# Kernel tuning notes

Hardware: AMD Instinct MI355X
Metric: run time of the kernel (lower is better)

## Reference

```python
import jax, jax.numpy as jnp
import numpy as np

EMBED_DIM = 1024
NUM_HEADS = 16
HEAD_DIM = EMBED_DIM // NUM_HEADS
SCALE = HEAD_DIM ** (-0.5)


def setup_inputs() -> dict:
    key = jax.random.key(0)
    ks = jax.random.split(key, 8)
    B, Nq, Nkv, C = 2, 2048, 2048, EMBED_DIM
    s = C ** (-0.5)
    return {
        "q": jax.random.normal(ks[0], (B, Nq, C), dtype=jnp.float32),
        "kv": jax.random.normal(ks[1], (B, Nkv, C), dtype=jnp.float32),
        "w_q": jax.random.normal(ks[2], (C, C), dtype=jnp.float32) * s,
        "b_q": jnp.zeros((C,), dtype=jnp.float32),
        "w_kv": jax.random.normal(ks[3], (C, 2 * C), dtype=jnp.float32) * s,
        "b_kv": jnp.zeros((2 * C,), dtype=jnp.float32),
        "w_out": jax.random.normal(ks[4], (C, C), dtype=jnp.float32) * s,
        "b_out": jnp.zeros((C,), dtype=jnp.float32),
    }


def reference(q, kv, w_q, b_q, w_kv, b_kv, w_out, b_out):
    B, Nq, C = q.shape
    _, Nkv, _ = kv.shape
    H, D = NUM_HEADS, HEAD_DIM

    # q projection: (B, Nq, C) -> (B, H, Nq, D)
    qp = (q @ w_q + b_q).reshape(B, Nq, H, D).transpose(0, 2, 1, 3)

    # kv projection: (B, Nkv, 2C) -> (2, B, H, Nkv, D); '(two h d)' layout
    kvp = (kv @ w_kv + b_kv).reshape(B, Nkv, 2, H, D).transpose(2, 0, 3, 1, 4)
    kp, vp = kvp[0], kvp[1]

    # attention scores (B, H, Nq, Nkv), softmax over kv axis
    attn = jnp.einsum("bhqd,bhkd->bhqk", qp, kp) * SCALE
    attn = jax.nn.softmax(attn, axis=-1)

    out = jnp.einsum("bhqk,bhkd->bhqd", attn, vp)
    out = out.transpose(0, 2, 1, 3).reshape(B, Nq, C)
    return out @ w_out + b_out
```

## Files before the change

kernel.cpp:

```cpp
#include <hip/hip_runtime.h>

#define NUM_HEADS 16
#define HEAD_DIM 64
#define EMBED 1024
#define SPLIT 2

typedef __attribute__((ext_vector_type(8))) short short8;
typedef __attribute__((ext_vector_type(4))) short short4v;
typedef __attribute__((ext_vector_type(4))) float f32x4;

#if __has_builtin(__builtin_amdgcn_exp2f)
#define EXP2F(x) __builtin_amdgcn_exp2f(x)
#else
#define EXP2F(x) exp2f(x)
#endif

__device__ __forceinline__ f32x4 mfma16_bf16(short4v a, short4v b, f32x4 c) {
#if defined(__HIP_DEVICE_COMPILE__)
  return __builtin_amdgcn_mfma_f32_16x16x16bf16_1k(a, b, c, 0, 0, 0);
#else
  return c;
#endif
}

__device__ __forceinline__ short f2bf(float f) {
  unsigned u = __builtin_bit_cast(unsigned, f);
  u += 0x7fffu + ((u >> 16) & 1u);
  return (short)(u >> 16);
}

__device__ __forceinline__ short f2bf_trunc(float f) {
  return (short)(__builtin_bit_cast(unsigned, f) >> 16);
}

__device__ __forceinline__ void gload_lds16(const void* g, void* l) {
  __builtin_amdgcn_global_load_lds(
      (const __attribute__((address_space(1))) void*)g,
      (__attribute__((address_space(3))) void*)l,
      16, 0, 0);
}

__device__ __forceinline__ void tr_body(const float* __restrict__ in,
                                        short* __restrict__ out, int R, int C,
                                        int bx, int by, float (*t)[33], int tid) {
  int tx = tid & 31, ty = tid >> 5;
#pragma unroll
  for (int i = 0; i < 32; i += 8)
    t[ty + i][tx] = in[(size_t)(by + ty + i) * C + bx + tx];
  __syncthreads();
#pragma unroll
  for (int i = 0; i < 32; i += 8)
    out[(size_t)(bx + ty + i) * R + by + tx] = f2bf(t[tx][ty + i]);
}

__global__ void prep(const float* __restrict__ q, short* __restrict__ q_bf,
                     const float* __restrict__ kv, short* __restrict__ kv_bf,
                     const float* __restrict__ w_q, short* __restrict__ wqt,
                     const float* __restrict__ w_kv, short* __restrict__ wkvt,
                     const float* __restrict__ w_out, short* __restrict__ wot) {
  __shared__ float t[32][33];
  int bid = blockIdx.x, tid = threadIdx.x;
  if (bid < 4096) {
    const float* in = bid < 2048 ? q : kv;
    short* out = bid < 2048 ? q_bf : kv_bf;
    int i = ((bid & 2047) * 256 + tid) * 8;
    float4 f0 = *(const float4*)(in + i);
    float4 f1 = *(const float4*)(in + i + 4);
    short8 r;
    r[0] = f2bf(f0.x); r[1] = f2bf(f0.y); r[2] = f2bf(f0.z); r[3] = f2bf(f0.w);
    r[4] = f2bf(f1.x); r[5] = f2bf(f1.y); r[6] = f2bf(f1.z); r[7] = f2bf(f1.w);
    *(short8*)(out + i) = r;
  } else if (bid < 5120) {
    int r = bid - 4096;
    tr_body(w_q, wqt, 1024, 1024, (r & 31) * 32, (r >> 5) * 32, t, tid);
  } else if (bid < 7168) {
    int r = bid - 5120;
    tr_body(w_kv, wkvt, 1024, 2048, (r & 63) * 32, (r >> 6) * 32, t, tid);
  } else {
    int r = bid - 7168;
    tr_body(w_out, wot, 1024, 1024, (r & 31) * 32, (r >> 5) * 32, t, tid);
  }
}

template <int MODE>
__device__ __forceinline__ void gemm_body(const short* __restrict__ A,
                                          const short* __restrict__ Bt,
                                          const float* __restrict__ bias,
                                          void* __restrict__ Cptr, int N, int K,
                                          int m0, int n0, float scale) {
  __shared__ short As[128 * 32];
  __shared__ short Bs[128 * 32];
  const int tid = threadIdx.x;
  const int wave = tid >> 6, lane = tid & 63;
  const int quad = lane >> 4, l16 = lane & 15;
  const int wr = wave >> 1, wc = wave & 1;

  f32x4 acc[4][4];
#pragma unroll
  for (int i = 0; i < 4; i++)
#pragma unroll
    for (int j = 0; j < 4; j++) acc[i][j] = (f32x4)0.f;

  const int c0 = wave * 2, c1 = wave * 2 + 1;
  const int rowA0 = c0 * 16 + (lane >> 2);
  const int rowA1 = c1 * 16 + (lane >> 2);
  const int kecol = (lane & 3) * 8;

  for (int k0 = 0; k0 < K; k0 += 32) {
    __syncthreads();
    gload_lds16(A + (size_t)(m0 + rowA0) * K + k0 + kecol, (char*)As + c0 * 1024);
    gload_lds16(A + (size_t)(m0 + rowA1) * K + k0 + kecol, (char*)As + c1 * 1024);
    gload_lds16(Bt + (size_t)(n0 + rowA0) * K + k0 + kecol, (char*)Bs + c0 * 1024);
    gload_lds16(Bt + (size_t)(n0 + rowA1) * K + k0 + kecol, (char*)Bs + c1 * 1024);
    __syncthreads();
    short8 a[4], b[4];
#pragma unroll
    for (int i = 0; i < 4; i++)
      a[i] = *(const short8*)(As + (wr * 64 + i * 16 + l16) * 32 + quad * 8);
#pragma unroll
    for (int j = 0; j < 4; j++)
      b[j] = *(const short8*)(Bs + (wc * 64 + j * 16 + l16) * 32 + quad * 8);
#pragma unroll
    for (int i = 0; i < 4; i++)
#pragma unroll
      for (int j = 0; j < 4; j++)
        acc[i][j] = __builtin_amdgcn_mfma_f32_16x16x32_bf16(a[i], b[j], acc[i][j], 0, 0, 0);
  }

#pragma unroll
  for (int j = 0; j < 4; j++) {
    int col = n0 + wc * 64 + j * 16 + l16;
    float bv = bias[col];
    if (MODE == 2) {
      int vcol = col - 1024;
      int h = vcol >> 6, d = vcol & 63;
#pragma unroll
      for (int i = 0; i < 4; i++) {
        int rbase = m0 + wr * 64 + i * 16 + quad * 4;
        int b = rbase >> 11;
        int kvr = rbase & 2047;
        short pk[4];
#pragma unroll
        for (int r = 0; r < 4; r++) pk[r] = f2bf(acc[i][j][r] + bv);
        *(uint2*)((short*)Cptr + ((size_t)(b * 16 + h) * 64 + d) * 2048 + kvr) =
            *(uint2*)pk;
      }
    } else {
#pragma unroll
      for (int i = 0; i < 4; i++) {
        int rbase = m0 + wr * 64 + i * 16 + quad * 4;
#pragma unroll
        for (int r = 0; r < 4; r++) {
          float v = (acc[i][j][r] + bv) * scale;
          if (MODE == 1)
            ((float*)Cptr)[(size_t)(rbase + r) * N + col] = v;
          else
            ((short*)Cptr)[(size_t)(rbase + r) * N + col] = f2bf(v);
        }
      }
    }
  }
}

__global__ __launch_bounds__(256)
void gemm_qkv(const short* __restrict__ q_bf, const short* __restrict__ kv_bf,
              const short* __restrict__ wqt, const short* __restrict__ wkvt,
              const float* __restrict__ b_q, const float* __restrict__ b_kv,
              short* __restrict__ qp, short* __restrict__ kvp,
              short* __restrict__ vt) {
  int y = blockIdx.y;
  int m0 = blockIdx.x * 128;
  if (y < 8) {
    gemm_body<0>(q_bf, wqt, b_q, qp, 1024, 1024, m0, y * 128, 0.125f);
  } else if (y < 16) {
    gemm_body<0>(kv_bf, wkvt, b_kv, kvp, 2048, 1024, m0, (y - 8) * 128, 1.f);
  } else {
    gemm_body<2>(kv_bf, wkvt, b_kv, vt, 2048, 1024, m0, (y - 8) * 128, 1.f);
  }
}

__global__ __launch_bounds__(256)
void gemm_out(const short* __restrict__ A, const short* __restrict__ Bt,
              const float* __restrict__ bias, float* __restrict__ C) {
  gemm_body<1>(A, Bt, bias, C, 1024, 1024, blockIdx.x * 128, blockIdx.y * 128, 1.f);
}

__global__ __launch_bounds__(256)
void attn7(const short* __restrict__ qp, const short* __restrict__ kvp,
           const short* __restrict__ vt, float* __restrict__ opart,
           float* __restrict__ lpart, int B, int Nq, int Nkv) {
  __shared__ short Ks0[64 * 64], Ks1[64 * 64];
  __shared__ short Vs0[64 * 64], Vs1[64 * 64];

  const int tid = threadIdx.x;
  const int wave = tid >> 6, lane = tid & 63;
  const int quad = lane >> 4, l16 = lane & 15;
  const int bh = blockIdx.y;
  const int b = bh >> 4, h = bh & 15;
  const int q0 = blockIdx.x * 64;
  const int z = blockIdx.z;
  const int kvlen = Nkv / SPLIT;
  const int kv_begin = z * kvlen;
  const int niter = kvlen / 64;

  const int qrow = q0 + wave * 16 + l16;
  const short* qbase = qp + ((size_t)b * Nq + qrow) * EMBED + h * HEAD_DIM;
  short8 aq0 = *(const short8*)(qbase + quad * 8);
  short8 aq1 = *(const short8*)(qbase + 32 + quad * 8);

  const int rl = lane >> 3;
  const int co = (lane & 7) ^ (rl & 7);
  const short* kgbase = kvp + (size_t)b * Nkv * 2048 + h * HEAD_DIM;
  const short* vgbase = vt + (size_t)(b * 16 + h) * 64 * 2048;

  f32x4 acc[4];
#pragma unroll
  for (int nt = 0; nt < 4; nt++) acc[nt] = (f32x4)0.f;
  float lsum = 0.f;

  const int swz_r = quad ^ (l16 & 7);
  const int swz_r4 = (quad + 4) ^ (l16 & 7);

  auto stage = [&](int it, short* Kd, short* Vd) {
    int kv0 = kv_begin + it * 64;
    gload_lds16(kgbase + (size_t)(kv0 + wave * 16 + rl) * 2048 + co * 8,
                Kd + wave * 1024);
    gload_lds16(kgbase + (size_t)(kv0 + wave * 16 + 8 + rl) * 2048 + co * 8,
                Kd + wave * 1024 + 512);
    gload_lds16(vgbase + (size_t)(wave * 16 + rl) * 2048 + kv0 + co * 8,
                Vd + wave * 1024);
    gload_lds16(vgbase + (size_t)(wave * 16 + 8 + rl) * 2048 + kv0 + co * 8,
                Vd + wave * 1024 + 512);
  };

  auto compute = [&](const short* Kt, const short* Vt_) {
    f32x4 s[4];
#pragma unroll
    for (int jt = 0; jt < 4; jt++) s[jt] = (f32x4)0.f;
#pragma unroll
    for (int jt = 0; jt < 4; ++jt) {
      const short* kr = Kt + (jt * 16 + l16) * 64;
      short8 ka0 = *(const short8*)(kr + swz_r * 8);
      short8 ka1 = *(const short8*)(kr + swz_r4 * 8);
      s[jt] = __builtin_amdgcn_mfma_f32_16x16x32_bf16(ka0, aq0, s[jt], 0, 0, 0);
      s[jt] = __builtin_amdgcn_mfma_f32_16x16x32_bf16(ka1, aq1, s[jt], 0, 0, 0);
    }
    short4v pf[4];
#pragma unroll
    for (int jt = 0; jt < 4; ++jt) {
      float e0 = EXP2F(__builtin_fmaf(s[jt][0], 1.44269504f, -17.3123405f));
      float e1 = EXP2F(__builtin_fmaf(s[jt][1], 1.44269504f, -17.3123405f));
      float e2 = EXP2F(__builtin_fmaf(s[jt][2], 1.44269504f, -17.3123405f));
      float e3 = EXP2F(__builtin_fmaf(s[jt][3], 1.44269504f, -17.3123405f));
      lsum += (e0 + e1) + (e2 + e3);
      short4v p;
      p[0] = f2bf_trunc(e0); p[1] = f2bf_trunc(e1);
      p[2] = f2bf_trunc(e2); p[3] = f2bf_trunc(e3);
      pf[jt] = p;
    }
#pragma unroll
    for (int jt = 0; jt < 4; ++jt) {
      const int chs = ((jt * 2 + (quad >> 1)) ^ (l16 & 7)) * 8 + (quad & 1) * 4;
#pragma unroll
      for (int nt = 0; nt < 4; ++nt) {
        short4v va = *(const short4v*)(Vt_ + (nt * 16 + l16) * 64 + chs);
        acc[nt] = mfma16_bf16(va, pf[jt], acc[nt]);
      }
    }
  };

  stage(0, Ks0, Vs0);
  for (int it = 0; it < niter; it += 2) {
    __syncthreads();
    stage(min(it + 1, niter - 1), Ks1, Vs1);
    compute(Ks0, Vs0);
    __syncthreads();
    stage(min(it + 2, niter - 1), Ks0, Vs0);
    compute(Ks1, Vs1);
  }

  lsum += __shfl_xor(lsum, 16);
  lsum += __shfl_xor(lsum, 32);
  const int qg = q0 + wave * 16 + l16;
  size_t obase = ((size_t)z * (B * Nq) + (size_t)b * Nq + qg) * EMBED + h * HEAD_DIM;
#pragma unroll
  for (int nt = 0; nt < 4; ++nt) {
    f32x4 v = acc[nt];
    float4 o = {v[0], v[1], v[2], v[3]};
    *(float4*)(opart + obase + nt * 16 + quad * 4) = o;
  }
  if (quad == 0) lpart[((size_t)z * 32 + bh) * 2048 + qg] = lsum;
}

__global__ void combine(const float* __restrict__ opart, const float* __restrict__ lpart,
                        short* __restrict__ aout, int Mq) {
  int i = (blockIdx.x * 256 + threadIdx.x) * 4;
  int row = i >> 10, c = i & 1023;
  int b = row >> 11, h = c >> 6;
  int qrow = row & 2047;
  float l0 = lpart[(size_t)(b * 16 + h) * 2048 + qrow];
  float l1 = lpart[((size_t)32 + b * 16 + h) * 2048 + qrow];
  float inv = 1.f / (l0 + l1);
  float4 o0 = *(const float4*)(opart + i);
  float4 o1 = *(const float4*)(opart + (size_t)Mq * 1024 + i);
  short r[4];
  r[0] = f2bf((o0.x + o1.x) * inv);
  r[1] = f2bf((o0.y + o1.y) * inv);
  r[2] = f2bf((o0.z + o1.z) * inv);
  r[3] = f2bf((o0.w + o1.w) * inv);
  *(uint2*)(aout + i) = *(uint2*)r;
}

extern "C" void kernel_launch(void* const* d_in, const int* in_sizes, int n_in,
                              void* d_out, int out_size, void* d_ws, size_t ws_size,
                              hipStream_t stream) {
  const float* q = (const float*)d_in[0];
  const float* kv = (const float*)d_in[1];
  const float* w_q = (const float*)d_in[2];
  const float* b_q = (const float*)d_in[3];
  const float* w_kv = (const float*)d_in[4];
  const float* b_kv = (const float*)d_in[5];
  const float* w_out = (const float*)d_in[6];
  const float* b_out = (const float*)d_in[7];

  const int B = 2, Nq = 2048, Nkv = 2048, C = 1024;
  const int Mq = B * Nq;

  char* ws = (char*)d_ws;
  short* qp = (short*)ws;
  short* kvp = qp + (size_t)Mq * C;
  short* vt = kvp + (size_t)Mq * 2 * C;
  short* aout = vt + (size_t)Mq * C;
  short* wot = aout + (size_t)Mq * C;
  float* lpart = (float*)(wot + (size_t)C * C);
  float* opart = lpart + (size_t)SPLIT * 32 * 2048;
  short* q_bf = (short*)opart;
  short* kv_bf = q_bf + (size_t)Mq * C;
  short* wqt = kv_bf + (size_t)Mq * C;
  short* wkvt = wqt + (size_t)C * C;

  prep<<<8192, 256, 0, stream>>>(q, q_bf, kv, kv_bf, w_q, wqt, w_kv, wkvt, w_out, wot);
  gemm_qkv<<<dim3(Mq / 128, 24), 256, 0, stream>>>(q_bf, kv_bf, wqt, wkvt, b_q, b_kv,
                                                   qp, kvp, vt);
  attn7<<<dim3(Nq / 64, B * NUM_HEADS, SPLIT), 256, 0, stream>>>(
      qp, kvp, vt, opart, lpart, B, Nq, Nkv);
  combine<<<Mq * 1024 / 4 / 256, 256, 0, stream>>>(opart, lpart, aout, Mq);
  gemm_out<<<dim3(Mq / 128, C / 128), 256, 0, stream>>>(aout, wot, b_out, (float*)d_out);
}
```

Before: 233.0 us.

## Shrink GEMM M-tile to 64 and store attention partials in bf16

The projection and output GEMMs now use 64x128 tiles instead of 128x128, doubling the block count and halving per-thread accumulators. This is meant to improve occupancy and wave count on the many-CU GPU. The split-KV attention partial outputs are now written and read as bf16 rather than fp32, which halves the traffic between attn7 and combine. The costs are less data reuse per tile and extra rounding on the unnormalized partial sums.

After: 230.9 us. Within noise of the previous version (-0.9%).

```diff
diff --git a/kernel.cpp b/kernel.cpp
--- a/kernel.cpp
+++ b/kernel.cpp
@@ -31,6 +31,11 @@
 
 __device__ __forceinline__ short f2bf_trunc(float f) {
   return (short)(__builtin_bit_cast(unsigned, f) >> 16);
+}
+
+__device__ __forceinline__ float bf2f(short s) {
+  unsigned u = ((unsigned)(unsigned short)s) << 16;
+  return __builtin_bit_cast(float, u);
 }
 
 __device__ __forceinline__ void gload_lds16(const void* g, void* l) {
@@ -83,45 +88,45 @@
 }
 
 template <int MODE>
-__device__ __forceinline__ void gemm_body(const short* __restrict__ A,
+__device__ __forceinline__ void gemm_body(short* As, short* Bs,
+                                          const short* __restrict__ A,
                                           const short* __restrict__ Bt,
                                           const float* __restrict__ bias,
                                           void* __restrict__ Cptr, int N, int K,
                                           int m0, int n0, float scale) {
-  __shared__ short As[128 * 32];
-  __shared__ short Bs[128 * 32];
   const int tid = threadIdx.x;
   const int wave = tid >> 6, lane = tid & 63;
   const int quad = lane >> 4, l16 = lane & 15;
   const int wr = wave >> 1, wc = wave & 1;
 
-  f32x4 acc[4][4];
-#pragma unroll
-  for (int i = 0; i < 4; i++)
+  f32x4 acc[2][4];
+#pragma unroll
+  for (int i = 0; i < 2; i++)
 #pragma unroll
     for (int j = 0; j < 4; j++) acc[i][j] = (f32x4)0.f;
 
+  const int rgrp = lane >> 2;
+  const int kecol = (lane & 3) * 8;
+  const int rowA = wave * 16 + rgrp;
   const int c0 = wave * 2, c1 = wave * 2 + 1;
-  const int rowA0 = c0 * 16 + (lane >> 2);
-  const int rowA1 = c1 * 16 + (lane >> 2);
-  const int kecol = (lane & 3) * 8;
+  const int rowB0 = c0 * 16 + rgrp;
+  const int rowB1 = c1 * 16 + rgrp;
 
   for (int k0 = 0; k0 < K; k0 += 32) {
     __syncthreads();
-    gload_lds16(A + (size_t)(m0 + rowA0) * K + k0 + kecol, (char*)As + c0 * 1024);
-    gload_lds16(A + (size_t)(m0 + rowA1) * K + k0 + kecol, (char*)As + c1 * 1024);
-    gload_lds16(Bt + (size_t)(n0 + rowA0) * K + k0 + kecol, (char*)Bs + c0 * 1024);
-    gload_lds16(Bt + (size_t)(n0 + rowA1) * K + k0 + kecol, (char*)Bs + c1 * 1024);
+    gload_lds16(A + (size_t)(m0 + rowA) * K + k0 + kecol, (char*)As + wave * 1024);
+    gload_lds16(Bt + (size_t)(n0 + rowB0) * K + k0 + kecol, (char*)Bs + c0 * 1024);
+    gload_lds16(Bt + (size_t)(n0 + rowB1) * K + k0 + kecol, (char*)Bs + c1 * 1024);
     __syncthreads();
-    short8 a[4], b[4];
-#pragma unroll
-    for (int i = 0; i < 4; i++)
-      a[i] = *(const short8*)(As + (wr * 64 + i * 16 + l16) * 32 + quad * 8);
+    short8 a[2], b[4];
+#pragma unroll
+    for (int i = 0; i < 2; i++)
+      a[i] = *(const short8*)(As + (wr * 32 + i * 16 + l16) * 32 + quad * 8);
 #pragma unroll
     for (int j = 0; j < 4; j++)
       b[j] = *(const short8*)(Bs + (wc * 64 + j * 16 + l16) * 32 + quad * 8);
 #pragma unroll
-    for (int i = 0; i < 4; i++)
+    for (int i = 0; i < 2; i++)
 #pragma unroll
       for (int j = 0; j < 4; j++)
         acc[i][j] = __builtin_amdgcn_mfma_f32_16x16x32_bf16(a[i], b[j], acc[i][j], 0, 0, 0);
@@ -135,8 +140,8 @@
       int vcol = col - 1024;
       int h = vcol >> 6, d = vcol & 63;
 #pragma unroll
-      for (int i = 0; i < 4; i++) {
-        int rbase = m0 + wr * 64 + i * 16 + quad * 4;
+      for (int i = 0; i < 2; i++) {
+        int rbase = m0 + wr * 32 + i * 16 + quad * 4;
         int b = rbase >> 11;
         int kvr = rbase & 2047;
         short pk[4];
@@ -147,8 +152,8 @@
       }
     } else {
 #pragma unroll
-      for (int i = 0; i < 4; i++) {
-        int rbase = m0 + wr * 64 + i * 16 + quad * 4;
+      for (int i = 0; i < 2; i++) {
+        int rbase = m0 + wr * 32 + i * 16 + quad * 4;
 #pragma unroll
         for (int r = 0; r < 4; r++) {
           float v = (acc[i][j][r] + bv) * scale;
@@ -168,26 +173,31 @@
               const float* __restrict__ b_q, const float* __restrict__ b_kv,
               short* __restrict__ qp, short* __restrict__ kvp,
               short* __restrict__ vt) {
+  __shared__ short As[64 * 32];
+  __shared__ short Bs[128 * 32];
   int y = blockIdx.y;
-  int m0 = blockIdx.x * 128;
+  int m0 = blockIdx.x * 64;
   if (y < 8) {
-    gemm_body<0>(q_bf, wqt, b_q, qp, 1024, 1024, m0, y * 128, 0.125f);
+    gemm_body<0>(As, Bs, q_bf, wqt, b_q, qp, 1024, 1024, m0, y * 128, 0.125f);
   } else if (y < 16) {
-    gemm_body<0>(kv_bf, wkvt, b_kv, kvp, 2048, 1024, m0, (y - 8) * 128, 1.f);
+    gemm_body<0>(As, Bs, kv_bf, wkvt, b_kv, kvp, 2048, 1024, m0, (y - 8) * 128, 1.f);
   } else {
-    gemm_body<2>(kv_bf, wkvt, b_kv, vt, 2048, 1024, m0, (y - 8) * 128, 1.f);
+    gemm_body<2>(As, Bs, kv_bf, wkvt, b_kv, vt, 2048, 1024, m0, (y - 8) * 128, 1.f);
   }
 }
 
 __global__ __launch_bounds__(256)
 void gemm_out(const short* __restrict__ A, const short* __restrict__ Bt,
               const float* __restrict__ bias, float* __restrict__ C) {
-  gemm_body<1>(A, Bt, bias, C, 1024, 1024, blockIdx.x * 128, blockIdx.y * 128, 1.f);
+  __shared__ short As[64 * 32];
+  __shared__ short Bs[128 * 32];
+  gemm_body<1>(As, Bs, A, Bt, bias, C, 1024, 1024, blockIdx.x * 64,
+               blockIdx.y * 128, 1.f);
 }
 
 __global__ __launch_bounds__(256)
 void attn7(const short* __restrict__ qp, const short* __restrict__ kvp,
-           const short* __restrict__ vt, float* __restrict__ opart,
+           const short* __restrict__ vt, short* __restrict__ opart,
            float* __restrict__ lpart, int B, int Nq, int Nkv) {
   __shared__ short Ks0[64 * 64], Ks1[64 * 64];
   __shared__ short Vs0[64 * 64], Vs1[64 * 64];
@@ -285,14 +295,15 @@
   size_t obase = ((size_t)z * (B * Nq) + (size_t)b * Nq + qg) * EMBED + h * HEAD_DIM;
 #pragma unroll
   for (int nt = 0; nt < 4; ++nt) {
-    f32x4 v = acc[nt];
-    float4 o = {v[0], v[1], v[2], v[3]};
-    *(float4*)(opart + obase + nt * 16 + quad * 4) = o;
+    short pk[4];
+#pragma unroll
+    for (int r = 0; r < 4; ++r) pk[r] = f2bf(acc[nt][r]);
+    *(uint2*)(opart + obase + nt * 16 + quad * 4) = *(uint2*)pk;
   }
   if (quad == 0) lpart[((size_t)z * 32 + bh) * 2048 + qg] = lsum;
 }
 
-__global__ void combine(const float* __restrict__ opart, const float* __restrict__ lpart,
+__global__ void combine(const short* __restrict__ opart, const float* __restrict__ lpart,
                         short* __restrict__ aout, int Mq) {
   int i = (blockIdx.x * 256 + threadIdx.x) * 4;
   int row = i >> 10, c = i & 1023;
@@ -301,13 +312,13 @@
   float l0 = lpart[(size_t)(b * 16 + h) * 2048 + qrow];
   float l1 = lpart[((size_t)32 + b * 16 + h) * 2048 + qrow];
   float inv = 1.f / (l0 + l1);
-  float4 o0 = *(const float4*)(opart + i);
-  float4 o1 = *(const float4*)(opart + (size_t)Mq * 1024 + i);
-  short r[4];
-  r[0] = f2bf((o0.x + o1.x) * inv);
-  r[1] = f2bf((o0.y + o1.y) * inv);
-  r[2] = f2bf((o0.z + o1.z) * inv);
-  r[3] = f2bf((o0.w + o1.w) * inv);
+  uint2 a0 = *(const uint2*)(opart + i);
+  uint2 a1 = *(const uint2*)(opart + (size_t)Mq * 1024 + i);
+  short s0[4], s1[4], r[4];
+  *(uint2*)s0 = a0;
+  *(uint2*)s1 = a1;
+#pragma unroll
+  for (int k = 0; k < 4; ++k) r[k] = f2bf((bf2f(s0[k]) + bf2f(s1[k])) * inv);
   *(uint2*)(aout + i) = *(uint2*)r;
 }
 
@@ -333,17 +344,17 @@
   short* aout = vt + (size_t)Mq * C;
   short* wot = aout + (size_t)Mq * C;
   float* lpart = (float*)(wot + (size_t)C * C);
-  float* opart = lpart + (size_t)SPLIT * 32 * 2048;
-  short* q_bf = (short*)opart;
+  short* opart = (short*)(lpart + (size_t)SPLIT * 32 * 2048);
+  short* q_bf = opart;
   short* kv_bf = q_bf + (size_t)Mq * C;
   short* wqt = kv_bf + (size_t)Mq * C;
   short* wkvt = wqt + (size_t)C * C;
 
   prep<<<8192, 256, 0, stream>>>(q, q_bf, kv, kv_bf, w_q, wqt, w_kv, wkvt, w_out, wot);
-  gemm_qkv<<<dim3(Mq / 128, 24), 256, 0, stream>>>(q_bf, kv_bf, wqt, wkvt, b_q, b_kv,
-                                                   qp, kvp, vt);
+  gemm_qkv<<<dim3(Mq / 64, 24), 256, 0, stream>>>(q_bf, kv_bf, wqt, wkvt, b_q, b_kv,
+                                                  qp, kvp, vt);
   attn7<<<dim3(Nq / 64, B * NUM_HEADS, SPLIT), 256, 0, stream>>>(
       qp, kvp, vt, opart, lpart, B, Nq, Nkv);
   combine<<<Mq * 1024 / 4 / 256, 256, 0, stream>>>(opart, lpart, aout, Mq);
-  gemm_out<<<dim3(Mq / 128, C / 128), 256, 0, stream>>>(aout, wot, b_out, (float*)d_out);
-}
+  gemm_out<<<dim3(Mq / 64, C / 128), 256, 0, stream>>>(aout, wot, b_out, (float*)d_out);
+}
```
